# Kernel optimization log

Hardware: AMD Instinct MI355X
Metric: run time of the kernel (lower is better)

Reference implementation:

```python
import jax, jax.numpy as jnp
import numpy as np

ISO = 0.0
# cube corner k has coords ((k>>0)&1, (k>>1)&1, (k>>2)&1)
CORNERS = np.array([[(k >> 0) & 1, (k >> 1) & 1, (k >> 2) & 1] for k in range(8)], np.int32)
# 6-tetrahedra decomposition of the cube around body diagonal 0-7
TETS = np.array([[0,1,3,7],[0,3,2,7],[0,2,6,7],[0,6,4,7],[0,4,5,7],[0,5,1,7]], np.int32)
TET_EDGES = np.array([[0,1],[0,2],[0,3],[1,2],[1,3],[2,3]], np.int32)
# marching-tetrahedra triangle table: sign case -> up to 2 triangles of tet-edge ids (-1 = pad)
MT_TRI = np.array([
 [-1,-1,-1,-1,-1,-1],
 [0,1,2,-1,-1,-1],
 [0,3,4,-1,-1,-1],
 [1,2,4,1,4,3],
 [1,3,5,-1,-1,-1],
 [0,2,5,0,5,3],
 [0,1,5,0,5,4],
 [2,4,5,-1,-1,-1],
 [2,4,5,-1,-1,-1],
 [0,1,5,0,5,4],
 [0,3,5,0,5,2],
 [1,3,5,-1,-1,-1],
 [1,3,4,1,4,2],
 [0,3,4,-1,-1,-1],
 [0,1,2,-1,-1,-1],
 [-1,-1,-1,-1,-1,-1]], np.int32)

# map (tet, tet-edge) -> unique per-cell edge slot; enumerate unique corner pairs
_pairs, _edges = {}, []
T2C = np.zeros((6, 6), np.int32)
for _ti in range(6):
    for _ei in range(6):
        _a = int(TETS[_ti, TET_EDGES[_ei, 0]]); _b = int(TETS[_ti, TET_EDGES[_ei, 1]])
        _key = (min(_a, _b), max(_a, _b))
        if _key not in _pairs:
            _pairs[_key] = len(_edges); _edges.append(_key)
        T2C[_ti, _ei] = _pairs[_key]
CELL_EDGES = np.array(_edges, np.int32)  # (19, 2)
N_EDGE = len(_edges)


def _forward(sdfsgrid, featgrid, isovalue=ISO):
    X, Y, Z = sdfsgrid.shape
    F = featgrid.shape[-1]
    dt = sdfsgrid.dtype
    # pad like the torch wrapper: sdf border = isovalue+1 (outside), features = 0
    s = jnp.pad(sdfsgrid, 1, constant_values=isovalue + 1.0)
    f = jnp.pad(featgrid, ((1, 1), (1, 1), (1, 1), (0, 0)))
    cx, cy, cz = s.shape[0] - 1, s.shape[1] - 1, s.shape[2] - 1
    # per-cell corner values: (cx,cy,cz,8) and (cx,cy,cz,8,F)
    cs = jnp.stack([s[dx:dx + cx, dy:dy + cy, dz:dz + cz] for dx, dy, dz in CORNERS], axis=-1)
    cf = jnp.stack([f[dx:dx + cx, dy:dy + cy, dz:dz + cz] for dx, dy, dz in CORNERS], axis=-2)
    inside = cs < isovalue
    ea, eb = CELL_EDGES[:, 0], CELL_EDGES[:, 1]
    sa, sb = cs[..., ea], cs[..., eb]                      # (cx,cy,cz,19)
    cross = inside[..., ea] != inside[..., eb]
    t = jnp.where(cross, (isovalue - sa) / jnp.where(cross, sb - sa, 1.0), 0.0)
    base = jnp.stack(jnp.meshgrid(jnp.arange(cx), jnp.arange(cy), jnp.arange(cz), indexing='ij'), axis=-1).astype(dt)
    pa = base[..., None, :] + jnp.asarray(CORNERS[ea], dt)  # (.,19,3)
    pb = base[..., None, :] + jnp.asarray(CORNERS[eb], dt)
    verts = pa + t[..., None] * (pb - pa)
    fa = jnp.take(cf, ea, axis=3)
    fb = jnp.take(cf, eb, axis=3)
    feats = fa + t[..., None] * (fb - fa)                  # (.,19,F)
    verts = jnp.where(cross[..., None], verts, 0.0)
    feats = jnp.where(cross[..., None], feats, 0.0)
    # triangles: per-tet sign case, table lookup, remap to per-cell edge slots
    bits = inside[..., TETS].astype(jnp.int32)             # (.,6,4)
    case = bits[..., 0] + 2 * bits[..., 1] + 4 * bits[..., 2] + 8 * bits[..., 3]
    ltri = jnp.asarray(MT_TRI)[case]                       # (.,6,6)
    ce = jnp.asarray(T2C)[jnp.arange(6)[:, None], jnp.clip(ltri, 0)]
    cell_lin = jnp.arange(cx * cy * cz, dtype=jnp.int32).reshape(cx, cy, cz)
    gid = jnp.where(ltri >= 0, cell_lin[..., None, None] * N_EDGE + ce, -1)
    tris = gid.reshape(-1, 3).astype(jnp.int32)
    scale = jnp.asarray([X, Y, Z], dt) - 1.0
    verts = (verts.reshape(-1, 3) - 1.0) / scale           # undo pad offset, normalize
    feats = feats.reshape(-1, F)
    return verts, feats, tris


def setup_inputs() -> dict:
    key = jax.random.key(0)
    k1, k2 = jax.random.split(key)
    sdfsgrid = jax.random.normal(k1, (64, 64, 64), jnp.float32)
    featgrid = jax.random.normal(k2, (64, 64, 64, 8), jnp.float32)
    return {"sdfsgrid": sdfsgrid, "featgrid": featgrid}


def reference(sdfsgrid, featgrid):
    return _forward(sdfsgrid, featgrid)
```

## Files before the change

kernel.cpp:

```cpp
#include <hip/hip_runtime.h>

#define NC 65
#define NCELL 274625
#define NE 19
#define NF 8

__constant__ unsigned MTP[16] = {
    0x00FFFFFFu, 0x00FFF210u, 0x00FFF430u, 0x00341421u,
    0x00FFF531u, 0x00350520u, 0x00450510u, 0x00FFF542u,
    0x00FFF542u, 0x00450510u, 0x00250530u, 0x00FFF531u,
    0x00241431u, 0x00FFF430u, 0x00FFF210u, 0x00FFFFFFu
};

__constant__ unsigned T2CPc[6] = {
    0x0A418820u, 0x105388C1u, 0x16850926u,
    0x1CB68989u, 0x22E809ECu, 0x0919080Fu
};

__device__ constexpr int EA[NE] = {0,0,0,1,1,3,0,2,2,0,2,6,0,4,4,0,4,5,1};
__device__ constexpr int EB[NE] = {1,3,7,3,7,7,2,3,7,6,6,7,4,6,7,5,5,7,5};
#define EAP 0x006C120C82419200ULL
#define EBP 0x017DBF4FB76BF7D9ULL
#define TETP 0x36C9B24D9ULL

typedef float float4u __attribute__((ext_vector_type(4), aligned(4)));
typedef float float2u __attribute__((ext_vector_type(2), aligned(4)));

#define LSTR 11

extern "C" __global__ void __launch_bounds__(256, 4)
diffmc_kernel(const float* __restrict__ sdf, const float* __restrict__ feat,
              float* __restrict__ oV, float* __restrict__ oF, float* __restrict__ oT)
{
    __shared__ float lds[256 * LSTR];
    const int tid = threadIdx.x;

    const int nwg = gridDim.x;
    const int q = nwg >> 3, r = nwg & 7;
    const int xcd = blockIdx.x & 7, s = blockIdx.x >> 3;
    const int swz = xcd * q + (xcd < r ? xcd : r) + s;

    const int blockBase = swz << 8;
    int vc = NCELL - blockBase;
    vc = vc > 256 ? 256 : vc;

    if (tid < vc) {
        const int cell = blockBase + tid;
        const int k  = cell % NC;
        const int t_ = cell / NC;
        const int j  = t_ % NC;
        const int i  = t_ / NC;
        float cs[8];
#pragma unroll
        for (int c = 0; c < 8; ++c) {
            int x = i + (c & 1) - 1;
            int y = j + ((c >> 1) & 1) - 1;
            int z = k + ((c >> 2) & 1) - 1;
            bool inb = ((unsigned)x < 64u) & ((unsigned)y < 64u) & ((unsigned)z < 64u);
            cs[c] = inb ? sdf[(x * 64 + y) * 64 + z] : 1.0f;
        }
        unsigned ins = 0;
#pragma unroll
        for (int c = 0; c < 8; ++c) ins |= (cs[c] < 0.0f ? 1u : 0u) << c;
        float* Ld = lds + tid * LSTR;
#pragma unroll
        for (int c = 0; c < 8; ++c) Ld[c] = cs[c];
        Ld[8] = __uint_as_float(ins);
        Ld[9] = __uint_as_float((unsigned)i | ((unsigned)j << 7) | ((unsigned)k << 14));
    }
    __syncthreads();

    const float inv63 = 1.0f / 63.0f;
    const int nE = vc * NE;
    const int nT = vc * 6;

    {
        float* __restrict__ dV = oV + (size_t)blockBase * 57;
        float* __restrict__ dF = oF + (size_t)blockBase * 152;
#pragma unroll 2
        for (int rr = 0; rr < 19; ++rr) {
            const int E = tid + (rr << 8);
            if (E >= nE) break;
            const unsigned c = (unsigned)E / 19u;
            const unsigned e = (unsigned)E - c * 19u;
            const float* Ld = lds + c * LSTR;
            const unsigned meta = __float_as_uint(Ld[9]);
            const unsigned ii = meta & 127u;
            const unsigned jj = (meta >> 7) & 127u;
            const unsigned kk = (meta >> 14) & 127u;
            const unsigned a = (unsigned)(EAP >> (3u * e)) & 7u;
            const unsigned b = (unsigned)(EBP >> (3u * e)) & 7u;
            const float sa = Ld[a], sb = Ld[b];
            const bool cross = (sa < 0.0f) != (sb < 0.0f);
            const float t = cross ? sa / (sa - sb) : 0.0f;

            const float pax = (float)(int)(ii + (a & 1u));
            const float pbx = (float)(int)(ii + (b & 1u));
            const float pay = (float)(int)(jj + ((a >> 1) & 1u));
            const float pby = (float)(int)(jj + ((b >> 1) & 1u));
            const float paz = (float)(int)(kk + ((a >> 2) & 1u));
            const float pbz = (float)(int)(kk + ((b >> 2) & 1u));
            const float vx = cross ? pax + t * (pbx - pax) : 0.0f;
            const float vy = cross ? pay + t * (pby - pay) : 0.0f;
            const float vz = cross ? paz + t * (pbz - paz) : 0.0f;
            const size_t vo = (size_t)E * 3u;
            dV[vo + 0] = (vx - 1.0f) * inv63;
            dV[vo + 1] = (vy - 1.0f) * inv63;
            dV[vo + 2] = (vz - 1.0f) * inv63;

            const int xa = (int)ii + (int)(a & 1u) - 1;
            const int ya = (int)jj + (int)((a >> 1) & 1u) - 1;
            const int za = (int)kk + (int)((a >> 2) & 1u) - 1;
            const int xb = (int)ii + (int)(b & 1u) - 1;
            const int yb = (int)jj + (int)((b >> 1) & 1u) - 1;
            const int zb = (int)kk + (int)((b >> 2) & 1u) - 1;
            const bool iba = ((unsigned)xa < 64u) & ((unsigned)ya < 64u) & ((unsigned)za < 64u);
            const bool ibb = ((unsigned)xb < 64u) & ((unsigned)yb < 64u) & ((unsigned)zb < 64u);
            float4 fa0 = make_float4(0.f, 0.f, 0.f, 0.f), fa1 = fa0;
            float4 fb0 = fa0, fb1 = fa0;
            if (iba) {
                const float4* fp = (const float4*)(feat + (size_t)((xa * 64 + ya) * 64 + za) * NF);
                fa0 = fp[0]; fa1 = fp[1];
            }
            if (ibb) {
                const float4* fp = (const float4*)(feat + (size_t)((xb * 64 + yb) * 64 + zb) * NF);
                fb0 = fp[0]; fb1 = fp[1];
            }
            float4u flo, fhi;
            flo.x = cross ? fa0.x + t * (fb0.x - fa0.x) : 0.0f;
            flo.y = cross ? fa0.y + t * (fb0.y - fa0.y) : 0.0f;
            flo.z = cross ? fa0.z + t * (fb0.z - fa0.z) : 0.0f;
            flo.w = cross ? fa0.w + t * (fb0.w - fa0.w) : 0.0f;
            fhi.x = cross ? fa1.x + t * (fb1.x - fa1.x) : 0.0f;
            fhi.y = cross ? fa1.y + t * (fb1.y - fa1.y) : 0.0f;
            fhi.z = cross ? fa1.z + t * (fb1.z - fa1.z) : 0.0f;
            fhi.w = cross ? fa1.w + t * (fb1.w - fa1.w) : 0.0f;
            const size_t fo = (size_t)E * 8u;
            *(float4u*)(dF + fo)     = flo;
            *(float4u*)(dF + fo + 4) = fhi;
        }
    }

    {
        float* __restrict__ dT = oT + (size_t)blockBase * 36;
#pragma unroll 2
        for (int rr = 0; rr < 6; ++rr) {
            const int T = tid + (rr << 8);
            if (T >= nT) break;
            const unsigned c  = (unsigned)T / 6u;
            const unsigned ti = (unsigned)T - c * 6u;
            const unsigned ins = __float_as_uint(lds[c * LSTR + 8]);
            const unsigned tc = (unsigned)(TETP >> (6u * ti)) & 63u;
            const unsigned c1 = tc & 7u, c2 = tc >> 3;
            const unsigned cse = (ins & 1u)
                               | (((ins >> c1) & 1u) << 1)
                               | (((ins >> c2) & 1u) << 2)
                               | (((ins >> 7) & 1u) << 3);
            const unsigned m  = MTP[cse];
            const unsigned tp = T2CPc[ti];
            const int cell19 = (blockBase + (int)c) * 19;
            float v6[6];
#pragma unroll
            for (int v = 0; v < 6; ++v) {
                const unsigned lt = (m >> (4 * v)) & 0xFu;
                const unsigned lc = (lt == 15u) ? 0u : lt;
                const unsigned ce = (tp >> (5 * lc)) & 31u;
                v6[v] = (lt == 15u) ? -1.0f : (float)(cell19 + (int)ce);
            }
            const size_t to = (size_t)T * 6u;
            float4u q0; q0.x = v6[0]; q0.y = v6[1]; q0.z = v6[2]; q0.w = v6[3];
            float2u q1; q1.x = v6[4]; q1.y = v6[5];
            *(float4u*)(dT + to)     = q0;
            *(float2u*)(dT + to + 4) = q1;
        }
    }
}

extern "C" void kernel_launch(void* const* d_in, const int* in_sizes, int n_in,
                              void* d_out, int out_size, void* d_ws, size_t ws_size,
                              hipStream_t stream) {
    const float* sdf  = (const float*)d_in[0];
    const float* feat = (const float*)d_in[1];
    float* out = (float*)d_out;
    float* oV = out;
    float* oF = oV + (size_t)NCELL * NE * 3;
    float* oT = oF + (size_t)NCELL * NE * NF;
    int blocks = (NCELL + 255) / 256;
    diffmc_kernel<<<blocks, 256, 0, stream>>>(sdf, feat, oV, oF, oT);
}
```

Baseline: 57.81 us.

## Split output writes into contiguous float4 streams per output array

Vertex, feature and triangle outputs are now written in separate loops. In each loop consecutive threads write consecutive float4 chunks, so stores coalesce, replacing the per-edge strided 3-float and 2x float4 stores. Vertex values are recomputed per component from LDS data, and the feature loop splits each edge into two half-vectors. The XCD block swizzle is also removed. This trades some extra index arithmetic and redundant interpolation work for better-coalesced global writes.

```diff
diff --git a/kernel.cpp b/kernel.cpp
--- a/kernel.cpp
+++ b/kernel.cpp
@@ -4,6 +4,7 @@
 #define NCELL 274625
 #define NE 19
 #define NF 8
+#define LSTR 11
 
 __constant__ unsigned MTP[16] = {
     0x00FFFFFFu, 0x00FFF210u, 0x00FFF430u, 0x00341421u,
@@ -11,12 +12,10 @@
     0x00FFF542u, 0x00450510u, 0x00250530u, 0x00FFF531u,
     0x00241431u, 0x00FFF430u, 0x00FFF210u, 0x00FFFFFFu
 };
-
 __constant__ unsigned T2CPc[6] = {
     0x0A418820u, 0x105388C1u, 0x16850926u,
     0x1CB68989u, 0x22E809ECu, 0x0919080Fu
 };
-
 __device__ constexpr int EA[NE] = {0,0,0,1,1,3,0,2,2,0,2,6,0,4,4,0,4,5,1};
 __device__ constexpr int EB[NE] = {1,3,7,3,7,7,2,3,7,6,6,7,4,6,7,5,5,7,5};
 #define EAP 0x006C120C82419200ULL
@@ -24,9 +23,25 @@
 #define TETP 0x36C9B24D9ULL
 
 typedef float float4u __attribute__((ext_vector_type(4), aligned(4)));
-typedef float float2u __attribute__((ext_vector_type(2), aligned(4)));
 
-#define LSTR 11
+__device__ __forceinline__ float vertVal(const float* lds, int P) {
+    const unsigned c    = (unsigned)P / 57u;
+    const unsigned rem  = (unsigned)P - c * 57u;
+    const unsigned e    = rem / 3u;
+    const unsigned comp = rem - e * 3u;
+    const float* Ld = lds + c * LSTR;
+    const unsigned meta = __float_as_uint(Ld[9]);
+    const unsigned a = (unsigned)(EAP >> (3u * e)) & 7u;
+    const unsigned b = (unsigned)(EBP >> (3u * e)) & 7u;
+    const float sa = Ld[a], sb = Ld[b];
+    const bool cross = (sa < 0.0f) != (sb < 0.0f);
+    const float t = cross ? sa / (sa - sb) : 0.0f;
+    const float coord = (float)(int)((meta >> (7u * comp)) & 127u);
+    const float pa = coord + (float)(int)((a >> comp) & 1u);
+    const float pb = coord + (float)(int)((b >> comp) & 1u);
+    const float v = cross ? pa + t * (pb - pa) : 0.0f;
+    return (v - 1.0f) * (1.0f / 63.0f);
+}
 
 extern "C" __global__ void __launch_bounds__(256, 4)
 diffmc_kernel(const float* __restrict__ sdf, const float* __restrict__ feat,
@@ -34,13 +49,7 @@
 {
     __shared__ float lds[256 * LSTR];
     const int tid = threadIdx.x;
-
-    const int nwg = gridDim.x;
-    const int q = nwg >> 3, r = nwg & 7;
-    const int xcd = blockIdx.x & 7, s = blockIdx.x >> 3;
-    const int swz = xcd * q + (xcd < r ? xcd : r) + s;
-
-    const int blockBase = swz << 8;
+    const int blockBase = blockIdx.x << 8;
     int vc = NCELL - blockBase;
     vc = vc > 256 ? 256 : vc;
 
@@ -70,108 +79,97 @@
     }
     __syncthreads();
 
-    const float inv63 = 1.0f / 63.0f;
-    const int nE = vc * NE;
-    const int nT = vc * 6;
+    {
+        const int nVd = vc * 57;
+        const int nV4 = nVd >> 2;
+        float* dV = oV + (size_t)blockBase * 57;
+        float4u* dV4 = (float4u*)dV;
+#pragma unroll 2
+        for (int rr = 0; rr < 15; ++rr) {
+            const int Q = tid + (rr << 8);
+            if (Q >= nV4) break;
+            float4u o;
+#pragma unroll
+            for (int u = 0; u < 4; ++u) o[u] = vertVal(lds, 4 * Q + u);
+            dV4[Q] = o;
+        }
+        const int tP = (nV4 << 2) + tid;
+        if (tP < nVd) dV[tP] = vertVal(lds, tP);
+    }
 
     {
-        float* __restrict__ dV = oV + (size_t)blockBase * 57;
-        float* __restrict__ dF = oF + (size_t)blockBase * 152;
+        const int nF4 = vc * 38;
+        float4u* dF4 = (float4u*)(oF + (size_t)blockBase * 152);
 #pragma unroll 2
-        for (int rr = 0; rr < 19; ++rr) {
-            const int E = tid + (rr << 8);
-            if (E >= nE) break;
-            const unsigned c = (unsigned)E / 19u;
-            const unsigned e = (unsigned)E - c * 19u;
+        for (int rr = 0; rr < 38; ++rr) {
+            const int Q = tid + (rr << 8);
+            if (Q >= nF4) break;
+            const unsigned c    = (unsigned)Q / 38u;
+            const unsigned rem  = (unsigned)Q - c * 38u;
+            const unsigned e    = rem >> 1;
+            const unsigned half = rem & 1u;
             const float* Ld = lds + c * LSTR;
             const unsigned meta = __float_as_uint(Ld[9]);
-            const unsigned ii = meta & 127u;
-            const unsigned jj = (meta >> 7) & 127u;
-            const unsigned kk = (meta >> 14) & 127u;
+            const int ii = (int)(meta & 127u);
+            const int jj = (int)((meta >> 7) & 127u);
+            const int kk = (int)((meta >> 14) & 127u);
             const unsigned a = (unsigned)(EAP >> (3u * e)) & 7u;
             const unsigned b = (unsigned)(EBP >> (3u * e)) & 7u;
             const float sa = Ld[a], sb = Ld[b];
             const bool cross = (sa < 0.0f) != (sb < 0.0f);
             const float t = cross ? sa / (sa - sb) : 0.0f;
 
-            const float pax = (float)(int)(ii + (a & 1u));
-            const float pbx = (float)(int)(ii + (b & 1u));
-            const float pay = (float)(int)(jj + ((a >> 1) & 1u));
-            const float pby = (float)(int)(jj + ((b >> 1) & 1u));
-            const float paz = (float)(int)(kk + ((a >> 2) & 1u));
-            const float pbz = (float)(int)(kk + ((b >> 2) & 1u));
-            const float vx = cross ? pax + t * (pbx - pax) : 0.0f;
-            const float vy = cross ? pay + t * (pby - pay) : 0.0f;
-            const float vz = cross ? paz + t * (pbz - paz) : 0.0f;
-            const size_t vo = (size_t)E * 3u;
-            dV[vo + 0] = (vx - 1.0f) * inv63;
-            dV[vo + 1] = (vy - 1.0f) * inv63;
-            dV[vo + 2] = (vz - 1.0f) * inv63;
-
-            const int xa = (int)ii + (int)(a & 1u) - 1;
-            const int ya = (int)jj + (int)((a >> 1) & 1u) - 1;
-            const int za = (int)kk + (int)((a >> 2) & 1u) - 1;
-            const int xb = (int)ii + (int)(b & 1u) - 1;
-            const int yb = (int)jj + (int)((b >> 1) & 1u) - 1;
-            const int zb = (int)kk + (int)((b >> 2) & 1u) - 1;
+            const int xa = ii + (int)(a & 1u) - 1;
+            const int ya = jj + (int)((a >> 1) & 1u) - 1;
+            const int za = kk + (int)((a >> 2) & 1u) - 1;
+            const int xb = ii + (int)(b & 1u) - 1;
+            const int yb = jj + (int)((b >> 1) & 1u) - 1;
+            const int zb = kk + (int)((b >> 2) & 1u) - 1;
             const bool iba = ((unsigned)xa < 64u) & ((unsigned)ya < 64u) & ((unsigned)za < 64u);
             const bool ibb = ((unsigned)xb < 64u) & ((unsigned)yb < 64u) & ((unsigned)zb < 64u);
-            float4 fa0 = make_float4(0.f, 0.f, 0.f, 0.f), fa1 = fa0;
-            float4 fb0 = fa0, fb1 = fa0;
-            if (iba) {
-                const float4* fp = (const float4*)(feat + (size_t)((xa * 64 + ya) * 64 + za) * NF);
-                fa0 = fp[0]; fa1 = fp[1];
-            }
-            if (ibb) {
-                const float4* fp = (const float4*)(feat + (size_t)((xb * 64 + yb) * 64 + zb) * NF);
-                fb0 = fp[0]; fb1 = fp[1];
-            }
-            float4u flo, fhi;
-            flo.x = cross ? fa0.x + t * (fb0.x - fa0.x) : 0.0f;
-            flo.y = cross ? fa0.y + t * (fb0.y - fa0.y) : 0.0f;
-            flo.z = cross ? fa0.z + t * (fb0.z - fa0.z) : 0.0f;
-            flo.w = cross ? fa0.w + t * (fb0.w - fa0.w) : 0.0f;
-            fhi.x = cross ? fa1.x + t * (fb1.x - fa1.x) : 0.0f;
-            fhi.y = cross ? fa1.y + t * (fb1.y - fa1.y) : 0.0f;
-            fhi.z = cross ? fa1.z + t * (fb1.z - fa1.z) : 0.0f;
-            fhi.w = cross ? fa1.w + t * (fb1.w - fa1.w) : 0.0f;
-            const size_t fo = (size_t)E * 8u;
-            *(float4u*)(dF + fo)     = flo;
-            *(float4u*)(dF + fo + 4) = fhi;
+            float4 fa = make_float4(0.f, 0.f, 0.f, 0.f), fb = fa;
+            if (iba) fa = *(const float4*)(feat + (size_t)((xa * 64 + ya) * 64 + za) * NF + 4 * half);
+            if (ibb) fb = *(const float4*)(feat + (size_t)((xb * 64 + yb) * 64 + zb) * NF + 4 * half);
+            float4u o;
+            o.x = cross ? fa.x + t * (fb.x - fa.x) : 0.0f;
+            o.y = cross ? fa.y + t * (fb.y - fa.y) : 0.0f;
+            o.z = cross ? fa.z + t * (fb.z - fa.z) : 0.0f;
+            o.w = cross ? fa.w + t * (fb.w - fa.w) : 0.0f;
+            dF4[Q] = o;
         }
     }
 
     {
-        float* __restrict__ dT = oT + (size_t)blockBase * 36;
+        const int nT4 = vc * 9;
+        float4u* dT4 = (float4u*)(oT + (size_t)blockBase * 36);
 #pragma unroll 2
-        for (int rr = 0; rr < 6; ++rr) {
-            const int T = tid + (rr << 8);
-            if (T >= nT) break;
-            const unsigned c  = (unsigned)T / 6u;
-            const unsigned ti = (unsigned)T - c * 6u;
+        for (int rr = 0; rr < 9; ++rr) {
+            const int Q = tid + (rr << 8);
+            if (Q >= nT4) break;
+            const unsigned c   = (unsigned)Q / 9u;
+            const unsigned rem = (unsigned)Q - c * 9u;
             const unsigned ins = __float_as_uint(lds[c * LSTR + 8]);
-            const unsigned tc = (unsigned)(TETP >> (6u * ti)) & 63u;
-            const unsigned c1 = tc & 7u, c2 = tc >> 3;
-            const unsigned cse = (ins & 1u)
-                               | (((ins >> c1) & 1u) << 1)
-                               | (((ins >> c2) & 1u) << 2)
-                               | (((ins >> 7) & 1u) << 3);
-            const unsigned m  = MTP[cse];
-            const unsigned tp = T2CPc[ti];
             const int cell19 = (blockBase + (int)c) * 19;
-            float v6[6];
+            float4u o;
 #pragma unroll
-            for (int v = 0; v < 6; ++v) {
-                const unsigned lt = (m >> (4 * v)) & 0xFu;
+            for (int u = 0; u < 4; ++u) {
+                const unsigned P  = 4u * rem + (unsigned)u;
+                const unsigned ti = P / 6u;
+                const unsigned v  = P - ti * 6u;
+                const unsigned tc = (unsigned)(TETP >> (6u * ti)) & 63u;
+                const unsigned c1 = tc & 7u, c2 = tc >> 3;
+                const unsigned cse = (ins & 1u)
+                                   | (((ins >> c1) & 1u) << 1)
+                                   | (((ins >> c2) & 1u) << 2)
+                                   | (((ins >> 7) & 1u) << 3);
+                const unsigned m  = MTP[cse];
+                const unsigned tp = T2CPc[ti];
+                const unsigned lt = (m >> (4u * v)) & 0xFu;
                 const unsigned lc = (lt == 15u) ? 0u : lt;
-                const unsigned ce = (tp >> (5 * lc)) & 31u;
-                v6[v] = (lt == 15u) ? -1.0f : (float)(cell19 + (int)ce);
+                const unsigned ce = (tp >> (5u * lc)) & 31u;
+                o[u] = (lt == 15u) ? -1.0f : (float)(cell19 + (int)ce);
             }
-            const size_t to = (size_t)T * 6u;
-            float4u q0; q0.x = v6[0]; q0.y = v6[1]; q0.z = v6[2]; q0.w = v6[3];
-            float2u q1; q1.x = v6[4]; q1.y = v6[5];
-            *(float4u*)(dT + to)     = q0;
-            *(float2u*)(dT + to + 4) = q1;
+            dT4[Q] = o;
         }
     }
 }
```

After: 74.04 us. 1.28x slower.

## Split kernel into three block roles for features, vertices and triangles

Applied to the files above, without the earlier changes.

Launches three times as many blocks, each assigned one output type (features, vertices, or triangle indices), instead of having every block write all three outputs. Every block still loads the sdf corners into shared memory, so that prologue is repeated three times. The XCD block-index swizzle is also removed. The goal is more parallelism and simpler per-block work on a store-bound kernel, at the cost of redundant sdf loads and unbalanced block durations.

```diff
diff --git a/kernel.cpp b/kernel.cpp
--- a/kernel.cpp
+++ b/kernel.cpp
@@ -4,6 +4,8 @@
 #define NCELL 274625
 #define NE 19
 #define NF 8
+#define LSTR 11
+#define NB 1073
 
 __constant__ unsigned MTP[16] = {
     0x00FFFFFFu, 0x00FFF210u, 0x00FFF430u, 0x00341421u,
@@ -11,12 +13,10 @@
     0x00FFF542u, 0x00450510u, 0x00250530u, 0x00FFF531u,
     0x00241431u, 0x00FFF430u, 0x00FFF210u, 0x00FFFFFFu
 };
-
 __constant__ unsigned T2CPc[6] = {
     0x0A418820u, 0x105388C1u, 0x16850926u,
     0x1CB68989u, 0x22E809ECu, 0x0919080Fu
 };
-
 __device__ constexpr int EA[NE] = {0,0,0,1,1,3,0,2,2,0,2,6,0,4,4,0,4,5,1};
 __device__ constexpr int EB[NE] = {1,3,7,3,7,7,2,3,7,6,6,7,4,6,7,5,5,7,5};
 #define EAP 0x006C120C82419200ULL
@@ -26,21 +26,15 @@
 typedef float float4u __attribute__((ext_vector_type(4), aligned(4)));
 typedef float float2u __attribute__((ext_vector_type(2), aligned(4)));
 
-#define LSTR 11
-
 extern "C" __global__ void __launch_bounds__(256, 4)
 diffmc_kernel(const float* __restrict__ sdf, const float* __restrict__ feat,
               float* __restrict__ oV, float* __restrict__ oF, float* __restrict__ oT)
 {
-    __shared__ float lds[256 * LSTR];
+    __shared__ float state[256 * LSTR];
     const int tid = threadIdx.x;
-
-    const int nwg = gridDim.x;
-    const int q = nwg >> 3, r = nwg & 7;
-    const int xcd = blockIdx.x & 7, s = blockIdx.x >> 3;
-    const int swz = xcd * q + (xcd < r ? xcd : r) + s;
-
-    const int blockBase = swz << 8;
+    const int role = blockIdx.x < NB ? 0 : (blockIdx.x < 2 * NB ? 1 : 2);
+    const int rbid = blockIdx.x - role * NB;
+    const int blockBase = rbid << 8;
     int vc = NCELL - blockBase;
     vc = vc > 256 ? 256 : vc;
 
@@ -62,7 +56,7 @@
         unsigned ins = 0;
 #pragma unroll
         for (int c = 0; c < 8; ++c) ins |= (cs[c] < 0.0f ? 1u : 0u) << c;
-        float* Ld = lds + tid * LSTR;
+        float* Ld = state + tid * LSTR;
 #pragma unroll
         for (int c = 0; c < 8; ++c) Ld[c] = cs[c];
         Ld[8] = __uint_as_float(ins);
@@ -71,107 +65,127 @@
     __syncthreads();
 
     const float inv63 = 1.0f / 63.0f;
-    const int nE = vc * NE;
-    const int nT = vc * 6;
-
-    {
-        float* __restrict__ dV = oV + (size_t)blockBase * 57;
+
+    if (role == 0) {
+        const int nE = vc * NE;
         float* __restrict__ dF = oF + (size_t)blockBase * 152;
 #pragma unroll 2
         for (int rr = 0; rr < 19; ++rr) {
             const int E = tid + (rr << 8);
-            if (E >= nE) break;
-            const unsigned c = (unsigned)E / 19u;
-            const unsigned e = (unsigned)E - c * 19u;
-            const float* Ld = lds + c * LSTR;
-            const unsigned meta = __float_as_uint(Ld[9]);
-            const unsigned ii = meta & 127u;
-            const unsigned jj = (meta >> 7) & 127u;
-            const unsigned kk = (meta >> 14) & 127u;
-            const unsigned a = (unsigned)(EAP >> (3u * e)) & 7u;
-            const unsigned b = (unsigned)(EBP >> (3u * e)) & 7u;
-            const float sa = Ld[a], sb = Ld[b];
-            const bool cross = (sa < 0.0f) != (sb < 0.0f);
-            const float t = cross ? sa / (sa - sb) : 0.0f;
-
-            const float pax = (float)(int)(ii + (a & 1u));
-            const float pbx = (float)(int)(ii + (b & 1u));
-            const float pay = (float)(int)(jj + ((a >> 1) & 1u));
-            const float pby = (float)(int)(jj + ((b >> 1) & 1u));
-            const float paz = (float)(int)(kk + ((a >> 2) & 1u));
-            const float pbz = (float)(int)(kk + ((b >> 2) & 1u));
-            const float vx = cross ? pax + t * (pbx - pax) : 0.0f;
-            const float vy = cross ? pay + t * (pby - pay) : 0.0f;
-            const float vz = cross ? paz + t * (pbz - paz) : 0.0f;
-            const size_t vo = (size_t)E * 3u;
-            dV[vo + 0] = (vx - 1.0f) * inv63;
-            dV[vo + 1] = (vy - 1.0f) * inv63;
-            dV[vo + 2] = (vz - 1.0f) * inv63;
-
-            const int xa = (int)ii + (int)(a & 1u) - 1;
-            const int ya = (int)jj + (int)((a >> 1) & 1u) - 1;
-            const int za = (int)kk + (int)((a >> 2) & 1u) - 1;
-            const int xb = (int)ii + (int)(b & 1u) - 1;
-            const int yb = (int)jj + (int)((b >> 1) & 1u) - 1;
-            const int zb = (int)kk + (int)((b >> 2) & 1u) - 1;
-            const bool iba = ((unsigned)xa < 64u) & ((unsigned)ya < 64u) & ((unsigned)za < 64u);
-            const bool ibb = ((unsigned)xb < 64u) & ((unsigned)yb < 64u) & ((unsigned)zb < 64u);
-            float4 fa0 = make_float4(0.f, 0.f, 0.f, 0.f), fa1 = fa0;
-            float4 fb0 = fa0, fb1 = fa0;
-            if (iba) {
-                const float4* fp = (const float4*)(feat + (size_t)((xa * 64 + ya) * 64 + za) * NF);
-                fa0 = fp[0]; fa1 = fp[1];
+            if (E < nE) {
+                const unsigned c = (unsigned)E / 19u;
+                const unsigned e = (unsigned)E - c * 19u;
+                const float* Ld = state + c * LSTR;
+                const unsigned meta = __float_as_uint(Ld[9]);
+                const int ii = (int)(meta & 127u);
+                const int jj = (int)((meta >> 7) & 127u);
+                const int kk = (int)((meta >> 14) & 127u);
+                const unsigned a = (unsigned)(EAP >> (3u * e)) & 7u;
+                const unsigned b = (unsigned)(EBP >> (3u * e)) & 7u;
+                const float sa = Ld[a], sb = Ld[b];
+                const bool cross = (sa < 0.0f) != (sb < 0.0f);
+                const float t = cross ? sa / (sa - sb) : 0.0f;
+
+                const int xa = ii + (int)(a & 1u) - 1;
+                const int ya = jj + (int)((a >> 1) & 1u) - 1;
+                const int za = kk + (int)((a >> 2) & 1u) - 1;
+                const int xb = ii + (int)(b & 1u) - 1;
+                const int yb = jj + (int)((b >> 1) & 1u) - 1;
+                const int zb = kk + (int)((b >> 2) & 1u) - 1;
+                const bool iba = ((unsigned)xa < 64u) & ((unsigned)ya < 64u) & ((unsigned)za < 64u);
+                const bool ibb = ((unsigned)xb < 64u) & ((unsigned)yb < 64u) & ((unsigned)zb < 64u);
+                float4 fa0 = make_float4(0.f, 0.f, 0.f, 0.f), fa1 = fa0;
+                float4 fb0 = fa0, fb1 = fa0;
+                if (iba) {
+                    const float4* fp = (const float4*)(feat + (size_t)((xa * 64 + ya) * 64 + za) * NF);
+                    fa0 = fp[0]; fa1 = fp[1];
+                }
+                if (ibb) {
+                    const float4* fp = (const float4*)(feat + (size_t)((xb * 64 + yb) * 64 + zb) * NF);
+                    fb0 = fp[0]; fb1 = fp[1];
+                }
+                float4u flo, fhi;
+                flo.x = cross ? fa0.x + t * (fb0.x - fa0.x) : 0.0f;
+                flo.y = cross ? fa0.y + t * (fb0.y - fa0.y) : 0.0f;
+                flo.z = cross ? fa0.z + t * (fb0.z - fa0.z) : 0.0f;
+                flo.w = cross ? fa0.w + t * (fb0.w - fa0.w) : 0.0f;
+                fhi.x = cross ? fa1.x + t * (fb1.x - fa1.x) : 0.0f;
+                fhi.y = cross ? fa1.y + t * (fb1.y - fa1.y) : 0.0f;
+                fhi.z = cross ? fa1.z + t * (fb1.z - fa1.z) : 0.0f;
+                fhi.w = cross ? fa1.w + t * (fb1.w - fa1.w) : 0.0f;
+                const size_t fo = (size_t)E * 8u;
+                *(float4u*)(dF + fo)     = flo;
+                *(float4u*)(dF + fo + 4) = fhi;
             }
-            if (ibb) {
-                const float4* fp = (const float4*)(feat + (size_t)((xb * 64 + yb) * 64 + zb) * NF);
-                fb0 = fp[0]; fb1 = fp[1];
+        }
+    } else if (role == 1) {
+        const int nE = vc * NE;
+        float* __restrict__ dV = oV + (size_t)blockBase * 57;
+#pragma unroll 2
+        for (int rr = 0; rr < 19; ++rr) {
+            const int E = tid + (rr << 8);
+            if (E < nE) {
+                const unsigned c = (unsigned)E / 19u;
+                const unsigned e = (unsigned)E - c * 19u;
+                const float* Ld = state + c * LSTR;
+                const unsigned meta = __float_as_uint(Ld[9]);
+                const unsigned ii = meta & 127u;
+                const unsigned jj = (meta >> 7) & 127u;
+                const unsigned kk = (meta >> 14) & 127u;
+                const unsigned a = (unsigned)(EAP >> (3u * e)) & 7u;
+                const unsigned b = (unsigned)(EBP >> (3u * e)) & 7u;
+                const float sa = Ld[a], sb = Ld[b];
+                const bool cross = (sa < 0.0f) != (sb < 0.0f);
+                const float t = cross ? sa / (sa - sb) : 0.0f;
+
+                const float pax = (float)(int)(ii + (a & 1u));
+                const float pbx = (float)(int)(ii + (b & 1u));
+                const float pay = (float)(int)(jj + ((a >> 1) & 1u));
+                const float pby = (float)(int)(jj + ((b >> 1) & 1u));
+                const float paz = (float)(int)(kk + ((a >> 2) & 1u));
+                const float pbz = (float)(int)(kk + ((b >> 2) & 1u));
+                const float vx = cross ? pax + t * (pbx - pax) : 0.0f;
+                const float vy = cross ? pay + t * (pby - pay) : 0.0f;
+                const float vz = cross ? paz + t * (pbz - paz) : 0.0f;
+                const size_t vo = (size_t)E * 3u;
+                dV[vo + 0] = (vx - 1.0f) * inv63;
+                dV[vo + 1] = (vy - 1.0f) * inv63;
+                dV[vo + 2] = (vz - 1.0f) * inv63;
             }
-            float4u flo, fhi;
-            flo.x = cross ? fa0.x + t * (fb0.x - fa0.x) : 0.0f;
-            flo.y = cross ? fa0.y + t * (fb0.y - fa0.y) : 0.0f;
-            flo.z = cross ? fa0.z + t * (fb0.z - fa0.z) : 0.0f;
-            flo.w = cross ? fa0.w + t * (fb0.w - fa0.w) : 0.0f;
-            fhi.x = cross ? fa1.x + t * (fb1.x - fa1.x) : 0.0f;
-            fhi.y = cross ? fa1.y + t * (fb1.y - fa1.y) : 0.0f;
-            fhi.z = cross ? fa1.z + t * (fb1.z - fa1.z) : 0.0f;
-            fhi.w = cross ? fa1.w + t * (fb1.w - fa1.w) : 0.0f;
-            const size_t fo = (size_t)E * 8u;
-            *(float4u*)(dF + fo)     = flo;
-            *(float4u*)(dF + fo + 4) = fhi;
-        }
-    }
-
-    {
+        }
+    } else {
+        const int nT = vc * 6;
         float* __restrict__ dT = oT + (size_t)blockBase * 36;
 #pragma unroll 2
         for (int rr = 0; rr < 6; ++rr) {
             const int T = tid + (rr << 8);
-            if (T >= nT) break;
-            const unsigned c  = (unsigned)T / 6u;
-            const unsigned ti = (unsigned)T - c * 6u;
-            const unsigned ins = __float_as_uint(lds[c * LSTR + 8]);
-            const unsigned tc = (unsigned)(TETP >> (6u * ti)) & 63u;
-            const unsigned c1 = tc & 7u, c2 = tc >> 3;
-            const unsigned cse = (ins & 1u)
-                               | (((ins >> c1) & 1u) << 1)
-                               | (((ins >> c2) & 1u) << 2)
-                               | (((ins >> 7) & 1u) << 3);
-            const unsigned m  = MTP[cse];
-            const unsigned tp = T2CPc[ti];
-            const int cell19 = (blockBase + (int)c) * 19;
-            float v6[6];
-#pragma unroll
-            for (int v = 0; v < 6; ++v) {
-                const unsigned lt = (m >> (4 * v)) & 0xFu;
-                const unsigned lc = (lt == 15u) ? 0u : lt;
-                const unsigned ce = (tp >> (5 * lc)) & 31u;
-                v6[v] = (lt == 15u) ? -1.0f : (float)(cell19 + (int)ce);
+            if (T < nT) {
+                const unsigned c  = (unsigned)T / 6u;
+                const unsigned ti = (unsigned)T - c * 6u;
+                const unsigned ins = __float_as_uint(state[c * LSTR + 8]);
+                const unsigned tc = (unsigned)(TETP >> (6u * ti)) & 63u;
+                const unsigned c1 = tc & 7u, c2 = tc >> 3;
+                const unsigned cse = (ins & 1u)
+                                   | (((ins >> c1) & 1u) << 1)
+                                   | (((ins >> c2) & 1u) << 2)
+                                   | (((ins >> 7) & 1u) << 3);
+                const unsigned m  = MTP[cse];
+                const unsigned tp = T2CPc[ti];
+                const int cell19 = (blockBase + (int)c) * 19;
+                float v6[6];
+#pragma unroll
+                for (int v = 0; v < 6; ++v) {
+                    const unsigned lt = (m >> (4 * v)) & 0xFu;
+                    const unsigned lc = (lt == 15u) ? 0u : lt;
+                    const unsigned ce = (tp >> (5 * lc)) & 31u;
+                    v6[v] = (lt == 15u) ? -1.0f : (float)(cell19 + (int)ce);
+                }
+                const size_t to = (size_t)T * 6u;
+                float4u q0; q0.x = v6[0]; q0.y = v6[1]; q0.z = v6[2]; q0.w = v6[3];
+                float2u q1; q1.x = v6[4]; q1.y = v6[5];
+                *(float4u*)(dT + to)     = q0;
+                *(float2u*)(dT + to + 4) = q1;
             }
-            const size_t to = (size_t)T * 6u;
-            float4u q0; q0.x = v6[0]; q0.y = v6[1]; q0.z = v6[2]; q0.w = v6[3];
-            float2u q1; q1.x = v6[4]; q1.y = v6[5];
-            *(float4u*)(dT + to)     = q0;
-            *(float2u*)(dT + to + 4) = q1;
         }
     }
 }
@@ -185,6 +199,5 @@
     float* oV = out;
     float* oF = oV + (size_t)NCELL * NE * 3;
     float* oT = oF + (size_t)NCELL * NE * NF;
-    int blocks = (NCELL + 255) / 256;
-    diffmc_kernel<<<blocks, 256, 0, stream>>>(sdf, feat, oV, oF, oT);
+    diffmc_kernel<<<3 * NB, 256, 0, stream>>>(sdf, feat, oV, oF, oT);
 }
```

Result: faster. 53.21 us (-8.0%).
